# Optimization experiments

Measured on AMD Instinct MI355X. Metric: run time of the kernel, lower is better.

The kernel has to match this reference:

```python
import jax, jax.numpy as jnp
import numpy as np

B, T, V, E, U = 64, 4995, 4096, 100, 64


def gru_layer(x, W, R, b, return_sequences):
    """Keras GRU (reset_after=True). x: [B,T,D]. Returns [B,T,U] or [B,U]."""
    u = R.shape[0]
    # Precompute all input projections in one big matmul: [B,T,3u]
    xp = jnp.einsum('btd,dk->btk', x, W) + b[0]
    h0 = jnp.zeros((x.shape[0], u), dtype=x.dtype)

    def step(h, xt):
        hp = h @ R + b[1]                                   # [B,3u]
        z = jax.nn.sigmoid(xt[:, :u] + hp[:, :u])
        r = jax.nn.sigmoid(xt[:, u:2 * u] + hp[:, u:2 * u])
        hh = jnp.tanh(xt[:, 2 * u:] + r * hp[:, 2 * u:])
        h_new = z * h + (1.0 - z) * hh
        return h_new, (h_new if return_sequences else None)

    hT, ys = jax.lax.scan(step, h0, jnp.swapaxes(xp, 0, 1))  # scan over time
    if return_sequences:
        return jnp.swapaxes(ys, 0, 1)                        # [B,T,U]
    return hT                                                # [B,U]


def setup_inputs() -> dict:
    key = jax.random.key(0)
    ks = jax.random.split(key, 8)
    s = 0.05
    return {
        'tokens': jax.random.randint(ks[0], (B, T), 0, V, dtype=jnp.int32),
        'emb': jax.random.normal(ks[1], (V, E), jnp.float32) * s,
        'W1': jax.random.normal(ks[2], (E, 3 * U), jnp.float32) * s,
        'U1': jax.random.normal(ks[3], (U, 3 * U), jnp.float32) * s,
        'b1': jnp.zeros((2, 3 * U), jnp.float32),
        'W2': jax.random.normal(ks[4], (U, 3 * U), jnp.float32) * s,
        'U2': jax.random.normal(ks[5], (U, 3 * U), jnp.float32) * s,
        'b2': jnp.zeros((2, 3 * U), jnp.float32),
        'Wout': jax.random.normal(ks[6], (U, 1), jnp.float32) * s,
        'bout': jnp.zeros((1,), jnp.float32),
    }


def reference(tokens, emb, W1, U1, b1, W2, U2, b2, Wout, bout):
    x = emb[tokens]                                   # [B,T,E] embedding lookup
    x = gru_layer(x, W1, U1, b1, return_sequences=True)   # [B,T,U]
    h = gru_layer(x, W2, U2, b2, return_sequences=False)  # [B,U] (last state)
    logits = h @ Wout + bout                          # [B,1]
    return jax.nn.sigmoid(logits)
```

## Files before the change

kernel.cpp:

```cpp
#include <hip/hip_runtime.h>

#define BB 64
#define TT 4995
#define VV 4096
#define EE 100
#define UU 64
#define U3 192
#define BPB 4
#define NBLK (BB / BPB)

using bf16x8 = __attribute__((ext_vector_type(8))) short;
using f32x4  = __attribute__((ext_vector_type(4))) float;

#define MFMA16 __builtin_amdgcn_mfma_f32_16x16x32_bf16

__device__ float g_embW[VV * U3];

__device__ __forceinline__ float fast_sigmoid(float x) {
    return __builtin_amdgcn_rcpf(1.0f + __expf(-x));
}
__device__ __forceinline__ float fast_tanh(float x) {
    return __builtin_amdgcn_rcpf(1.0f + __expf(-2.0f * x)) * 2.0f - 1.0f;
}
__device__ __forceinline__ unsigned short f2bf(float f) {
    unsigned u = __float_as_uint(f);
    return (unsigned short)((u + 0x7FFFu + ((u >> 16) & 1u)) >> 16);
}
__device__ __forceinline__ float bf2f(unsigned short h) {
    return __uint_as_float(((unsigned)h) << 16);
}

__global__ void gru_embw_kernel(const float* __restrict__ emb,
                                const float* __restrict__ W1,
                                const float* __restrict__ b1) {
    __shared__ float row[EE];
    const int v = blockIdx.x;
    const int k = threadIdx.x;
    if (k < EE) row[k] = emb[v * EE + k];
    __syncthreads();
    float acc = b1[k];
    #pragma unroll 4
    for (int j = 0; j < EE; ++j)
        acc = fmaf(row[j], W1[j * U3 + k], acc);
    g_embW[v * U3 + k] = acc;
}

__global__ __launch_bounds__(512, 1)
void gru_scan_kernel(const int* __restrict__ tokens,
                     const float* __restrict__ U1,
                     const float* __restrict__ b1,
                     const float* __restrict__ W2,
                     const float* __restrict__ U2,
                     const float* __restrict__ b2,
                     const float* __restrict__ Wout,
                     const float* __restrict__ bout,
                     float* __restrict__ out) {
    const int blk  = blockIdx.x;
    const int tid  = threadIdx.x;
    const int wave = tid >> 6;
    const int lane = tid & 63;
    const int lg   = lane >> 4;
    const int lc   = lane & 15;
    const bool isL2 = (wave >= 4);
    const int ut   = wave & 3;

    __shared__ __align__(16) char hls[8192];
    for (int i = tid; i < 2048; i += 512) ((int*)hls)[i] = 0;

    bf16x8 fb[12];
    const int cz = ut * 16 + lc;
    const int cr = 64 + ut * 16 + lc;
    const int ch = 128 + ut * 16 + lc;
    {
        const float* M0 = isL2 ? W2 : U1;
        #pragma unroll
        for (int g = 0; g < 3; ++g) {
            const int col = g * 64 + ut * 16 + lc;
            #pragma unroll
            for (int kk = 0; kk < 2; ++kk) {
                bf16x8 v;
                #pragma unroll
                for (int e = 0; e < 8; ++e)
                    v[e] = (short)f2bf(M0[(8 * lg + 32 * kk + e) * U3 + col]);
                fb[g * 2 + kk] = v;
            }
        }
        if (isL2) {
            #pragma unroll
            for (int g = 0; g < 3; ++g) {
                const int col = g * 64 + ut * 16 + lc;
                #pragma unroll
                for (int kk = 0; kk < 2; ++kk) {
                    bf16x8 v;
                    #pragma unroll
                    for (int e = 0; e < 8; ++e)
                        v[e] = (short)f2bf(U2[(8 * lg + 32 * kk + e) * U3 + col]);
                    fb[6 + g * 2 + kk] = v;
                }
            }
        } else {
            #pragma unroll
            for (int q = 6; q < 12; ++q) fb[q] = fb[q - 6];
        }
    }

    float bias_z, bias_r, bias_h, bias_h2 = 0.0f;
    if (!isL2) {
        bias_z = b1[U3 + cz]; bias_r = b1[U3 + cr]; bias_h = b1[U3 + ch];
    } else {
        bias_z  = b2[cz] + b2[U3 + cz];
        bias_r  = b2[cr] + b2[U3 + cr];
        bias_h  = b2[ch];
        bias_h2 = b2[U3 + ch];
    }
    const f32x4 bz4 = {bias_z, bias_z, bias_z, bias_z};
    const f32x4 br4 = {bias_r, bias_r, bias_r, bias_r};
    const f32x4 bh4 = {bias_h, bias_h, bias_h, bias_h};
    const f32x4 bp4 = {bias_h2, bias_h2, bias_h2, bias_h2};
    const f32x4 zq  = {0.0f, 0.0f, 0.0f, 0.0f};

    float xp[2][3];
    int   tok[2];
    const int rowbase = (blk * BPB + lg) * TT;
    if (!isL2) {
        const int t0 = tokens[rowbase];
        tok[0] = tokens[rowbase + 1];
        tok[1] = tokens[rowbase + 2];
        xp[0][0] = g_embW[t0 * U3 + cz];
        xp[0][1] = g_embW[t0 * U3 + cr];
        xp[0][2] = g_embW[t0 * U3 + ch];
    }

    float h1o = 0.0f;
    float h2o = 0.0f;

    __syncthreads();

    const int swzA = (lc & 7) << 4;
    const int myrow = 4 * lg;
    const int wswz  = ((myrow & 7) << 4);
    const int wbyte = myrow * 128 + (((ut * 16 + lc) * 2) ^ wswz);

    #pragma unroll 1
    for (int sb = 0; sb < TT + 1; sb += 2) {
        #pragma unroll
        for (int half = 0; half < 2; ++half) {
            const int s = sb + half;
            char* rdb = hls + half * 4096;
            char* wrb = hls + (half ^ 1) * 4096;

            if (!isL2) {
                const int tn = tok[half];
                xp[half ^ 1][0] = g_embW[tn * U3 + cz];
                xp[half ^ 1][1] = g_embW[tn * U3 + cr];
                xp[half ^ 1][2] = g_embW[tn * U3 + ch];
                const int s2 = (s + 2 < TT) ? (s + 2) : (TT - 1);
                tok[half ^ 1] = tokens[rowbase + s2];

                bf16x8 a1_0 = *(const bf16x8*)(rdb + lc * 128 + ((16 * lg) ^ swzA));
                bf16x8 a1_1 = *(const bf16x8*)(rdb + lc * 128 + ((16 * lg + 64) ^ swzA));

                if (s < TT) {
                    f32x4 az = MFMA16(a1_0, fb[0], bz4, 0, 0, 0);
                    az       = MFMA16(a1_1, fb[1], az,  0, 0, 0);
                    f32x4 ar = MFMA16(a1_0, fb[2], br4, 0, 0, 0);
                    ar       = MFMA16(a1_1, fb[3], ar,  0, 0, 0);
                    f32x4 ah = MFMA16(a1_0, fb[4], bh4, 0, 0, 0);
                    ah       = MFMA16(a1_1, fb[5], ah,  0, 0, 0);
                    const float z  = fast_sigmoid(xp[half][0] + az[0]);
                    const float rg = fast_sigmoid(xp[half][1] + ar[0]);
                    const float hh = fast_tanh(xp[half][2] + rg * ah[0]);
                    h1o = fmaf(z, h1o - hh, hh);
                    *(unsigned short*)(wrb + wbyte) = f2bf(h1o);
                }
            } else {
                bf16x8 a1_0 = *(const bf16x8*)(rdb + lc * 128 + ((16 * lg) ^ swzA));
                bf16x8 a1_1 = *(const bf16x8*)(rdb + lc * 128 + ((16 * lg + 64) ^ swzA));
                bf16x8 a2_0 = *(const bf16x8*)(rdb + 2048 + lc * 128 + ((16 * lg) ^ swzA));
                bf16x8 a2_1 = *(const bf16x8*)(rdb + 2048 + lc * 128 + ((16 * lg + 64) ^ swzA));

                if (s > 0) {
                    f32x4 az1 = MFMA16(a1_0, fb[0],  bz4, 0, 0, 0);
                    az1       = MFMA16(a1_1, fb[1],  az1, 0, 0, 0);
                    f32x4 az2 = MFMA16(a2_0, fb[6],  zq,  0, 0, 0);
                    az2       = MFMA16(a2_1, fb[7],  az2, 0, 0, 0);
                    f32x4 ar1 = MFMA16(a1_0, fb[2],  br4, 0, 0, 0);
                    ar1       = MFMA16(a1_1, fb[3],  ar1, 0, 0, 0);
                    f32x4 ar2 = MFMA16(a2_0, fb[8],  zq,  0, 0, 0);
                    ar2       = MFMA16(a2_1, fb[9],  ar2, 0, 0, 0);
                    f32x4 ax  = MFMA16(a1_0, fb[4],  bh4, 0, 0, 0);
                    ax        = MFMA16(a1_1, fb[5],  ax,  0, 0, 0);
                    f32x4 ap  = MFMA16(a2_0, fb[10], bp4, 0, 0, 0);
                    ap        = MFMA16(a2_1, fb[11], ap,  0, 0, 0);
                    const float z  = fast_sigmoid(az1[0] + az2[0]);
                    const float rg = fast_sigmoid(ar1[0] + ar2[0]);
                    const float hh = fast_tanh(ax[0] + rg * ap[0]);
                    h2o = fmaf(z, h2o - hh, hh);
                    *(unsigned short*)(wrb + 2048 + wbyte) = f2bf(h2o);
                }
            }
            __syncthreads();
        }
    }

    if (wave == 0 && lane < BPB) {
        const int row = 4 * lane;
        float acc = bout[0];
        #pragma unroll 8
        for (int u = 0; u < UU; ++u) {
            const unsigned short hv = *(const unsigned short*)(hls + 2048 +
                row * 128 + ((u * 2) ^ ((row & 7) << 4)));
            acc = fmaf(bf2f(hv), Wout[u], acc);
        }
        out[blk * BPB + lane] = fast_sigmoid(acc);
    }
}

extern "C" void kernel_launch(void* const* d_in, const int* in_sizes, int n_in,
                              void* d_out, int out_size, void* d_ws, size_t ws_size,
                              hipStream_t stream) {
    const int*   tokens = (const int*)  d_in[0];
    const float* emb    = (const float*)d_in[1];
    const float* W1     = (const float*)d_in[2];
    const float* U1w    = (const float*)d_in[3];
    const float* b1     = (const float*)d_in[4];
    const float* W2     = (const float*)d_in[5];
    const float* U2w    = (const float*)d_in[6];
    const float* b2     = (const float*)d_in[7];
    const float* Wout   = (const float*)d_in[8];
    const float* bout   = (const float*)d_in[9];
    float* out = (float*)d_out;

    gru_embw_kernel<<<VV, 192, 0, stream>>>(emb, W1, b1);
    gru_scan_kernel<<<NBLK, 512, 0, stream>>>(tokens, U1w, b1, W2, U2w,
                                              b2, Wout, bout, out);
}
```

Measured before the change: 1.649 ms.

## Deepen token/embedding prefetch to four steps and use LDS-only barrier

Swaps __syncthreads for a custom barrier that waits only on LDS counters (lgkmcnt), so outstanding global loads for the prefetched embedding rows need not drain at each step. The layer-1 token and embedding-projection prefetch is deepened from two steps ahead to four, with a 4-phase unrolled loop, to give global-memory latency more time to hide behind the serial recurrence. The cost is more registers and a riskier hand-written barrier whose correctness depends on the compiler inserting waits for the global loads before use.

```diff
diff --git a/kernel.cpp b/kernel.cpp
--- a/kernel.cpp
+++ b/kernel.cpp
@@ -13,6 +13,14 @@
 using f32x4  = __attribute__((ext_vector_type(4))) float;
 
 #define MFMA16 __builtin_amdgcn_mfma_f32_16x16x32_bf16
+
+#define LDS_BARRIER()                                   \
+    do {                                                \
+        __builtin_amdgcn_sched_barrier(0);              \
+        asm volatile("s_waitcnt lgkmcnt(0)" ::: "memory"); \
+        __builtin_amdgcn_s_barrier();                   \
+        __builtin_amdgcn_sched_barrier(0);              \
+    } while (0)
 
 __device__ float g_embW[VV * U3];
 
@@ -119,16 +127,24 @@
     const f32x4 bp4 = {bias_h2, bias_h2, bias_h2, bias_h2};
     const f32x4 zq  = {0.0f, 0.0f, 0.0f, 0.0f};
 
-    float xp[2][3];
-    int   tok[2];
+    float xp[4][3];
+    int   tok[4];
     const int rowbase = (blk * BPB + lg) * TT;
     if (!isL2) {
         const int t0 = tokens[rowbase];
-        tok[0] = tokens[rowbase + 1];
-        tok[1] = tokens[rowbase + 2];
+        const int t1 = tokens[rowbase + 1];
+        tok[2] = tokens[rowbase + 2];
+        tok[3] = tokens[rowbase + 3];
+        tok[0] = 0; tok[1] = 0;
         xp[0][0] = g_embW[t0 * U3 + cz];
         xp[0][1] = g_embW[t0 * U3 + cr];
         xp[0][2] = g_embW[t0 * U3 + ch];
+        xp[1][0] = g_embW[t1 * U3 + cz];
+        xp[1][1] = g_embW[t1 * U3 + cr];
+        xp[1][2] = g_embW[t1 * U3 + ch];
+        #pragma unroll
+        for (int q = 2; q < 4; ++q)
+            xp[q][0] = xp[q][1] = xp[q][2] = 0.0f;
     }
 
     float h1o = 0.0f;
@@ -142,20 +158,20 @@
     const int wbyte = myrow * 128 + (((ut * 16 + lc) * 2) ^ wswz);
 
     #pragma unroll 1
-    for (int sb = 0; sb < TT + 1; sb += 2) {
+    for (int sq = 0; sq < TT + 1; sq += 4) {
         #pragma unroll
-        for (int half = 0; half < 2; ++half) {
-            const int s = sb + half;
-            char* rdb = hls + half * 4096;
-            char* wrb = hls + (half ^ 1) * 4096;
+        for (int ph = 0; ph < 4; ++ph) {
+            const int s = sq + ph;
+            char* rdb = hls + (ph & 1) * 4096;
+            char* wrb = hls + ((ph & 1) ^ 1) * 4096;
 
             if (!isL2) {
-                const int tn = tok[half];
-                xp[half ^ 1][0] = g_embW[tn * U3 + cz];
-                xp[half ^ 1][1] = g_embW[tn * U3 + cr];
-                xp[half ^ 1][2] = g_embW[tn * U3 + ch];
-                const int s2 = (s + 2 < TT) ? (s + 2) : (TT - 1);
-                tok[half ^ 1] = tokens[rowbase + s2];
+                const int tn = tok[(ph + 2) & 3];
+                xp[(ph + 2) & 3][0] = g_embW[tn * U3 + cz];
+                xp[(ph + 2) & 3][1] = g_embW[tn * U3 + cr];
+                xp[(ph + 2) & 3][2] = g_embW[tn * U3 + ch];
+                const int s4 = (s + 4 < TT) ? (s + 4) : (TT - 1);
+                tok[ph & 3] = tokens[rowbase + s4];
 
                 bf16x8 a1_0 = *(const bf16x8*)(rdb + lc * 128 + ((16 * lg) ^ swzA));
                 bf16x8 a1_1 = *(const bf16x8*)(rdb + lc * 128 + ((16 * lg + 64) ^ swzA));
@@ -167,9 +183,9 @@
                     ar       = MFMA16(a1_1, fb[3], ar,  0, 0, 0);
                     f32x4 ah = MFMA16(a1_0, fb[4], bh4, 0, 0, 0);
                     ah       = MFMA16(a1_1, fb[5], ah,  0, 0, 0);
-                    const float z  = fast_sigmoid(xp[half][0] + az[0]);
-                    const float rg = fast_sigmoid(xp[half][1] + ar[0]);
-                    const float hh = fast_tanh(xp[half][2] + rg * ah[0]);
+                    const float z  = fast_sigmoid(xp[ph][0] + az[0]);
+                    const float rg = fast_sigmoid(xp[ph][1] + ar[0]);
+                    const float hh = fast_tanh(xp[ph][2] + rg * ah[0]);
                     h1o = fmaf(z, h1o - hh, hh);
                     *(unsigned short*)(wrb + wbyte) = f2bf(h1o);
                 }
@@ -199,7 +215,7 @@
                     *(unsigned short*)(wrb + 2048 + wbyte) = f2bf(h2o);
                 }
             }
-            __syncthreads();
+            LDS_BARRIER();
         }
     }
 
```

After: 1.645 ms. About the same (-0.3%).
